# Optimization experiments

Measured on AMD Instinct MI355X. Metric: run time of the kernel, lower is better.

The kernel has to match this reference:

```python
import jax, jax.numpy as jnp
import numpy as np

N0, N1, N2 = 200000, 50000, 10000
D_IN, D_PROMPT, D_HID, D_OUT = 128, 64, 256, 2
E0, E1 = 800000, 160000


def _glorot(key, shape):
    fan_in, fan_out = shape[0], shape[1]
    lim = np.sqrt(6.0 / (fan_in + fan_out))
    return jax.random.uniform(key, shape, jnp.float32, -lim, lim)


def setup_inputs() -> dict:
    key = jax.random.key(0)
    ks = jax.random.split(key, 20)
    inp = {
        "features": jax.random.normal(ks[0], (N0, D_IN), jnp.float32),
        "membership_mask": jax.random.randint(ks[1], (N0,), 0, 2) > 0,
        "src0": jax.random.randint(ks[2], (E0,), 0, N0),
        "dst0": jax.random.randint(ks[3], (E0,), 0, N1),
        "src1": jax.random.randint(ks[4], (E1,), 0, N1),
        "dst1": jax.random.randint(ks[5], (E1,), 0, N2),
        "output_nodes_indices": jax.random.randint(ks[6], (N2,), 0, N2),
        # prompt MLPs
        "w_pin": _glorot(ks[7], (D_IN, D_PROMPT)),
        "b_pin": jnp.zeros((D_PROMPT,), jnp.float32),
        "w_pout": _glorot(ks[8], (D_IN, D_PROMPT)),
        "b_pout": jnp.zeros((D_PROMPT,), jnp.float32),
        # SAGEConv layer 0: (D_IN+D_PROMPT) -> D_HID
        "w_self0": _glorot(ks[9], (D_IN + D_PROMPT, D_HID)),
        "w_neigh0": _glorot(ks[10], (D_IN + D_PROMPT, D_HID)),
        "b0": jnp.zeros((D_HID,), jnp.float32),
        # SAGEConv layer 1: D_HID -> D_HID
        "w_self1": _glorot(ks[11], (D_HID, D_HID)),
        "w_neigh1": _glorot(ks[12], (D_HID, D_HID)),
        "b1": jnp.zeros((D_HID,), jnp.float32),
        # classifier
        "w_cls": _glorot(ks[13], (D_HID, D_OUT)),
        "b_cls": jnp.zeros((D_OUT,), jnp.float32),
    }
    return inp


def _sage_mean(h, src, dst, n_dst, w_self, w_neigh, b):
    # mean-aggregate src features into dst buckets (zero-degree -> 0, DGL semantics)
    agg = jax.ops.segment_sum(h[src], dst, num_segments=n_dst)
    deg = jax.ops.segment_sum(jnp.ones((src.shape[0],), h.dtype), dst, num_segments=n_dst)
    agg = agg / jnp.maximum(deg, 1.0)[:, None]
    return h[:n_dst] @ w_self + agg @ w_neigh + b


def reference(features, membership_mask, src0, dst0, src1, dst1, output_nodes_indices,
              w_pin, b_pin, w_pout, b_pout,
              w_self0, w_neigh0, b0, w_self1, w_neigh1, b1, w_cls, b_cls):
    p_in = jax.nn.relu(features @ w_pin + b_pin)
    p_out = jax.nn.relu(features @ w_pout + b_pout)
    sel = jnp.where(membership_mask[:, None], p_in, p_out)
    h = jnp.concatenate([features, sel], axis=1)          # [N0, D_IN+D_PROMPT]
    h = jax.nn.relu(_sage_mean(h, src0, dst0, N1, w_self0, w_neigh0, b0))  # [N1, D_HID]
    h = _sage_mean(h, src1, dst1, N2, w_self1, w_neigh1, b1)               # [N2, D_HID]
    logits = h @ w_cls + b_cls                             # [N2, D_OUT]
    return logits
```

## Files before the change

kernel.cpp:

```cpp
#include <hip/hip_runtime.h>


#define N0v 200000
#define N1v 50000
#define N2v 10000
#define E0v 800000
#define E1v 160000
#define TB0 49
#define TB1 10
#define TBL (TB0 + TB1)

using u16 = unsigned short;
typedef __attribute__((ext_vector_type(8))) short short8;
typedef __attribute__((ext_vector_type(4))) float f32x4;

__device__ __forceinline__ float b2f(u16 u) {
    union { unsigned int i; float f; } v; v.i = ((unsigned int)u) << 16; return v.f;
}
__device__ __forceinline__ u16 f2b(float f) {
    union { float f; unsigned int i; } v; v.f = f;
    return (u16)((v.i + 0x7fffu + ((v.i >> 16) & 1u)) >> 16);
}
__device__ __forceinline__ void split2(float f, u16& h, u16& l) {
    h = f2b(f);
    l = f2b(f - b2f(h));
}

__global__ void k_prep(const unsigned* mask, int* flag,
                       const float* w_pin, const float* w_pout, u16* WTph, u16* WTpl,
                       const float* ws0, const float* wn0, u16* WT0h, u16* WT0l,
                       const float* ws1, const float* wn1, u16* WT1h, u16* WT1l,
                       const float* bc, float* outp,
                       const int* __restrict__ dst0, const int* __restrict__ dst1,
                       int* cnt0, int* cnt1) {
    const int R0 = 50000;
    const int R1 = R0 + 128 * 128;
    const int R2 = R1 + 256 * 384;
    const int R3 = R2 + 256 * 512;
    const int R4 = R3 + 2 * N2v;
    const int R5 = R4 + E0v;
    const int R6 = R5 + E1v;
    for (int i = blockIdx.x * blockDim.x + threadIdx.x; i < R6;
         i += gridDim.x * blockDim.x) {
        if (i < R0) {
            if (mask[i] > 1u) atomicOr(flag, 1);
        } else if (i < R1) {
            int j = i - R0, n = j >> 7, k = j & 127;
            float f = (n < 64) ? w_pin[k * 64 + n] : w_pout[k * 64 + (n - 64)];
            split2(f, WTph[j], WTpl[j]);
        } else if (i < R2) {
            int j = i - R1, n = j / 384, k = j % 384;
            float f = (k < 192) ? ws0[k * 256 + n] : wn0[(k - 192) * 256 + n];
            split2(f, WT0h[j], WT0l[j]);
        } else if (i < R3) {
            int j = i - R2, n = j >> 9, k = j & 511;
            float f = (k < 256) ? ws1[k * 256 + n] : wn1[(k - 256) * 256 + n];
            split2(f, WT1h[j], WT1l[j]);
        } else if (i < R4) {
            int j = i - R3;
            outp[j] = bc[j & 1];
        } else if (i < R5) {
            atomicAdd(&cnt0[dst0[i - R4]], 1);
        } else {
            atomicAdd(&cnt1[dst1[i - R5]], 1);
        }
    }
}

__global__ __launch_bounds__(256) void k_scan_a(const int* __restrict__ cnt0,
                                                int* __restrict__ off0,
                                                const int* __restrict__ cnt1,
                                                int* __restrict__ off1,
                                                int* __restrict__ tsum) {
    __shared__ int sd[256];
    const int t = threadIdx.x;
    const int blk = blockIdx.x;
    const int g1 = (blk >= TB0);
    const int b = g1 ? blk - TB0 : blk;
    const int n = g1 ? N2v : N1v;
    const int* cnt = g1 ? cnt1 : cnt0;
    int* off = g1 ? off1 : off0;
    const int i0 = b * 1024 + t * 4;
    int c[4] = {0, 0, 0, 0};
    if (i0 + 3 < n) {
        *(int4*)c = *(const int4*)&cnt[i0];
    } else {
        for (int j = 0; j < 4; j++) if (i0 + j < n) c[j] = cnt[i0 + j];
    }
    int s = c[0] + c[1] + c[2] + c[3];
    sd[t] = s;
    __syncthreads();
#pragma unroll
    for (int d = 1; d < 256; d <<= 1) {
        int v = (t >= d) ? sd[t - d] : 0;
        __syncthreads();
        sd[t] += v;
        __syncthreads();
    }
    int run = sd[t] - s;
    int o4[4];
#pragma unroll
    for (int j = 0; j < 4; j++) { o4[j] = run; run += c[j]; }
    if (i0 + 3 < n) *(int4*)&off[i0] = *(const int4*)o4;
    else for (int j = 0; j < 4; j++) if (i0 + j < n) off[i0 + j] = o4[j];
    if (t == 255) tsum[blk] = sd[255];
}

__global__ __launch_bounds__(256) void k_scan_c(int* __restrict__ off0,
                                                int* __restrict__ off1,
                                                const int* __restrict__ tsum) {
    __shared__ int lbase;
    const int t = threadIdx.x;
    const int blk = blockIdx.x;
    const int g1 = (blk >= TB0);
    const int b = g1 ? blk - TB0 : blk;
    const int n = g1 ? N2v : N1v;
    int* off = g1 ? off1 : off0;
    if (t < 64) {
        int v = (t < TBL) ? tsum[t] : 0;
        int incl = v;
#pragma unroll
        for (int d = 1; d < 64; d <<= 1) {
            int u = __shfl_up(incl, d);
            if (t >= d) incl += u;
        }
        int total0 = __shfl(incl, TB0 - 1);
        if (t == blk) lbase = (incl - v) - (g1 ? total0 : 0);
    }
    __syncthreads();
    const int base = lbase;
    const int i0 = b * 1024 + t * 4;
    if (i0 + 3 < n) {
        int4 v = *(int4*)&off[i0];
        v.x += base; v.y += base; v.z += base; v.w += base;
        *(int4*)&off[i0] = v;
    } else {
        for (int j = 0; j < 4; j++) if (i0 + j < n) off[i0 + j] += base;
    }
    if (blk == 0 && t == 0) { off0[N1v] = E0v; off1[N2v] = E1v; }
}

__global__ void k_scatter2(const int* __restrict__ src0, const int* __restrict__ dst0,
                           const int* __restrict__ off0, int* cur0, int* ei0,
                           const int* __restrict__ src1, const int* __restrict__ dst1,
                           const int* __restrict__ off1, int* cur1, int* ei1) {
    for (int i = blockIdx.x * blockDim.x + threadIdx.x; i < E0v + E1v;
         i += gridDim.x * blockDim.x) {
        if (i < E0v) {
            int d = dst0[i];
            ei0[off0[d] + atomicAdd(&cur0[d], 1)] = src0[i];
        } else {
            int d = dst1[i - E0v];
            ei1[off1[d] + atomicAdd(&cur1[d], 1)] = src1[i - E0v];
        }
    }
}

__global__ __launch_bounds__(256, 2) void k_gemm_p(
    const float* __restrict__ A, const u16* __restrict__ Bh, const u16* __restrict__ Bl,
    const float* __restrict__ b_pin, const float* __restrict__ b_pout,
    const void* maskp, const int* __restrict__ flag, u16* __restrict__ G) {
    __shared__ __align__(16) u16 LA[16 * 68 * 8];
    const int t = threadIdx.x;
    const int bm = blockIdx.x >> 1, bn = blockIdx.x & 1;
    const int lane = t & 63, w = t >> 6;
    const int m = lane & 15, q = lane >> 4;
    const int r0 = bm * 64;
    const int col = bn * 64 + w * 16 + m;

    short8 bf[4][2];
#pragma unroll
    for (int k0 = 0; k0 < 4; k0++) {
        size_t b = (size_t)col * 128 + k0 * 32 + q * 8;
        bf[k0][0] = *(const short8*)&Bh[b];
        bf[k0][1] = *(const short8*)&Bl[b];
    }

    {
        const int r15 = t >> 4, ch = t & 15;
        const int k0 = ch >> 2, q2 = ch & 3;
#pragma unroll
        for (int p = 0; p < 4; p++) {
            const int row = r0 + r15 + 16 * p;
            const float* ap = &A[(size_t)row * 128 + ch * 8];
            float4 v0 = *(const float4*)ap, v1 = *(const float4*)(ap + 4);
            u16 h8[8];
            h8[0] = f2b(v0.x); h8[1] = f2b(v0.y); h8[2] = f2b(v0.z); h8[3] = f2b(v0.w);
            h8[4] = f2b(v1.x); h8[5] = f2b(v1.y); h8[6] = f2b(v1.z); h8[7] = f2b(v1.w);
            if (bn == 0)
                *(uint4*)&G[(size_t)row * 192 + ch * 8] = *(const uint4*)h8;
            const int fi = p * 4 + k0, pos = 16 * q2 + r15;
            *(uint4*)&LA[(fi * 68 + pos) * 8] = *(const uint4*)h8;
        }
    }
    __syncthreads();

    f32x4 acc[4] = {};
#pragma unroll
    for (int mi = 0; mi < 4; mi++) {
#pragma unroll
        for (int k0 = 0; k0 < 4; k0++) {
            short8 af = *(const short8*)&LA[((mi * 4 + k0) * 68 + lane) * 8];
            acc[mi] = __builtin_amdgcn_mfma_f32_16x16x32_bf16(af, bf[k0][0], acc[mi], 0, 0, 0);
            acc[mi] = __builtin_amdgcn_mfma_f32_16x16x32_bf16(af, bf[k0][1], acc[mi], 0, 0, 0);
        }
    }

    const float bv = (col < 64) ? b_pin[col] : b_pout[col - 64];
    __syncthreads();
#pragma unroll
    for (int mi = 0; mi < 4; mi++) {
#pragma unroll
        for (int r = 0; r < 4; r++) {
            float v = acc[mi][r] + bv;
            v = v > 0.f ? v : 0.f;
            LA[(mi * 16 + q * 4 + r) * 72 + w * 16 + m] = f2b(v);
        }
    }
    __syncthreads();
    const int fl = *flag;
    {
        const int c8 = t & 7;
#pragma unroll
        for (int pass = 0; pass < 2; pass++) {
            const int rt = pass * 32 + (t >> 3);
            const int row = r0 + rt;
            bool mk = fl ? (((const unsigned char*)maskp)[row] != 0)
                         : (((const int*)maskp)[row] != 0);
            if (mk == (bn == 0)) {
                *(uint4*)&G[(size_t)row * 192 + 128 + c8 * 8] =
                    *(const uint4*)&LA[rt * 72 + c8 * 8];
            }
        }
    }
}

template <int MODE, int KT, int KE0, int MT>
__global__ __launch_bounds__(256, 2) void k_g(
    const u16* __restrict__ A0, int s0, const u16* __restrict__ A1, int s1,
    const u16* __restrict__ Bh, const u16* __restrict__ Bl,
    const float* __restrict__ bias,
    u16* __restrict__ CH, float* __restrict__ outp, const float* __restrict__ wc,
    int M) {
    constexpr int MI = MT / 16;
    __shared__ __align__(16) u16 LA[MI * KT * 68 * 8];
    const int t = threadIdx.x;
    const int bm = blockIdx.x >> 2, bn = blockIdx.x & 3;
    const int lane = t & 63, w = t >> 6;
    const int m = lane & 15, q = lane >> 4;
    const int r0 = bm * MT;
    const int col = bn * 64 + w * 16 + m;
    const int K = KT * 32;

    {
        constexpr int TPR = 256 / MT;
        constexpr int SPT = KT / TPR;
        const int rr = t / TPR, sub = t & (TPR - 1);
        int arow = r0 + rr; if (arow >= M) arow = M - 1;
        const int mi = rr >> 4, r15 = rr & 15;
#pragma unroll
        for (int s = 0; s < SPT; s++) {
            const int kc = sub * SPT + s;
#pragma unroll
            for (int q2 = 0; q2 < 4; q2++) {
                const int c = kc * 32 + q2 * 8;
                uint4 v = (c < KE0 * 32)
                              ? *(const uint4*)&A0[(size_t)arow * s0 + c]
                              : *(const uint4*)&A1[(size_t)arow * s1 + (c - KE0 * 32)];
                *(uint4*)&LA[((mi * KT + kc) * 68 + 16 * q2 + r15) * 8] = v;
            }
        }
    }
    __syncthreads();

    f32x4 acc[MI] = {};
#pragma unroll
    for (int kb = 0; kb < KT; kb += 8) {
        constexpr int KC8 = (KT < 8) ? KT : 8;
        const int KC = (KT - kb < KC8) ? (KT - kb) : KC8;
        short8 bf[KC8][2];
#pragma unroll
        for (int k0 = 0; k0 < KC8; k0++) {
            if (k0 < KC) {
                size_t b = (size_t)col * K + (kb + k0) * 32 + q * 8;
                bf[k0][0] = *(const short8*)&Bh[b];
                bf[k0][1] = *(const short8*)&Bl[b];
            }
        }
#pragma unroll
        for (int mi = 0; mi < MI; mi++) {
#pragma unroll
            for (int k0 = 0; k0 < KC8; k0++) {
                if (k0 < KC) {
                    short8 af = *(const short8*)&LA[((mi * KT + kb + k0) * 68 + lane) * 8];
                    acc[mi] = __builtin_amdgcn_mfma_f32_16x16x32_bf16(af, bf[k0][0], acc[mi], 0, 0, 0);
                    acc[mi] = __builtin_amdgcn_mfma_f32_16x16x32_bf16(af, bf[k0][1], acc[mi], 0, 0, 0);
                }
            }
        }
    }

    const float bv = bias[col];
    if (MODE == 1) {
        __syncthreads();
#pragma unroll
        for (int mi = 0; mi < MI; mi++) {
#pragma unroll
            for (int r = 0; r < 4; r++) {
                float v = acc[mi][r] + bv;
                v = v > 0.f ? v : 0.f;
                LA[(mi * 16 + q * 4 + r) * 72 + w * 16 + m] = f2b(v);
            }
        }
        __syncthreads();
        const int c8 = t & 7;
#pragma unroll
        for (int pass = 0; pass < MT / 32; pass++) {
            const int rt = pass * 32 + (t >> 3);
            const int row = r0 + rt;
            if (row < M) {
                *(uint4*)&CH[(size_t)row * 256 + bn * 64 + c8 * 8] =
                    *(const uint4*)&LA[rt * 72 + c8 * 8];
            }
        }
    } else {
        const float w0 = wc[col * 2], w1 = wc[col * 2 + 1];
#pragma unroll
        for (int mi = 0; mi < MI; mi++) {
#pragma unroll
            for (int r = 0; r < 4; r++) {
                int row = r0 + mi * 16 + q * 4 + r;
                float v = acc[mi][r] + bv;
                float p0 = v * w0, p1 = v * w1;
#pragma unroll
                for (int s = 1; s < 16; s <<= 1) {
                    p0 += __shfl_xor(p0, s);
                    p1 += __shfl_xor(p1, s);
                }
                if (m == 0 && row < M) {
                    atomicAdd(&outp[row * 2], p0);
                    atomicAdd(&outp[row * 2 + 1], p1);
                }
            }
        }
    }
}

__global__ void k_agg0(const u16* __restrict__ G, const int* __restrict__ off,
                       const int* __restrict__ eidx, u16* __restrict__ aggH) {
    int wid = (blockIdx.x * blockDim.x + threadIdx.x) >> 6;
    int lane = threadIdx.x & 63;
    if (wid >= N1v) return;
    int b = off[wid], e = off[wid + 1];
    float f0 = 0.f, f1 = 0.f, p0 = 0.f;
    for (int base = b; base < e; base += 64) {
        int li = base + lane;
        int idx = eidx[li < e ? li : (e - 1)];
        int nch = e - base; if (nch > 64) nch = 64;
        int j = 0;
        for (; j + 4 <= nch; j += 4) {
            int sa = __shfl(idx, j), sb = __shfl(idx, j + 1);
            int sc = __shfl(idx, j + 2), sd = __shfl(idx, j + 3);
            const u16* ra = &G[(size_t)sa * 192];
            const u16* rb = &G[(size_t)sb * 192];
            const u16* rc = &G[(size_t)sc * 192];
            const u16* rd = &G[(size_t)sd * 192];
            unsigned fa = *(const unsigned*)&ra[2 * lane];
            unsigned fb = *(const unsigned*)&rb[2 * lane];
            unsigned fc = *(const unsigned*)&rc[2 * lane];
            unsigned fd = *(const unsigned*)&rd[2 * lane];
            u16 pa = ra[128 + lane], pb = rb[128 + lane];
            u16 pc = rc[128 + lane], pd = rd[128 + lane];
            f0 += b2f((u16)fa) + b2f((u16)fb) + b2f((u16)fc) + b2f((u16)fd);
            f1 += b2f((u16)(fa >> 16)) + b2f((u16)(fb >> 16)) +
                  b2f((u16)(fc >> 16)) + b2f((u16)(fd >> 16));
            p0 += b2f(pa) + b2f(pb) + b2f(pc) + b2f(pd);
        }
        for (; j < nch; j++) {
            int s = __shfl(idx, j);
            const u16* row = &G[(size_t)s * 192];
            unsigned fv = *(const unsigned*)&row[2 * lane];
            f0 += b2f((u16)fv);
            f1 += b2f((u16)(fv >> 16));
            p0 += b2f(row[128 + lane]);
        }
    }
    int deg = e - b;
    float inv = 1.0f / (float)(deg > 1 ? deg : 1);
    size_t rb2 = (size_t)wid * 192;
    *(unsigned*)&aggH[rb2 + 2 * lane] =
        (unsigned)f2b(f0 * inv) | ((unsigned)f2b(f1 * inv) << 16);
    aggH[rb2 + 128 + lane] = f2b(p0 * inv);
}

__global__ void k_agg1(const u16* __restrict__ h1H, const int* __restrict__ off,
                       const int* __restrict__ eidx, u16* __restrict__ aggH) {
    int wid = (blockIdx.x * blockDim.x + threadIdx.x) >> 6;
    int lane = threadIdx.x & 63;
    if (wid >= N2v) return;
    int b = off[wid], e = off[wid + 1];
    float a0 = 0.f, a1 = 0.f, a2 = 0.f, a3 = 0.f;
    for (int base = b; base < e; base += 64) {
        int li = base + lane;
        int idx = eidx[li < e ? li : (e - 1)];
        int nch = e - base; if (nch > 64) nch = 64;
        int j = 0;
        for (; j + 4 <= nch; j += 4) {
            int sa = __shfl(idx, j), sb = __shfl(idx, j + 1);
            int sc = __shfl(idx, j + 2), sd = __shfl(idx, j + 3);
            const u16* ra = &h1H[(size_t)sa * 256];
            const u16* rb = &h1H[(size_t)sb * 256];
            const u16* rc = &h1H[(size_t)sc * 256];
            const u16* rd = &h1H[(size_t)sd * 256];
            unsigned va0 = *(const unsigned*)&ra[2 * lane];
            unsigned vb0 = *(const unsigned*)&rb[2 * lane];
            unsigned vc0 = *(const unsigned*)&rc[2 * lane];
            unsigned vd0 = *(const unsigned*)&rd[2 * lane];
            unsigned va1 = *(const unsigned*)&ra[128 + 2 * lane];
            unsigned vb1 = *(const unsigned*)&rb[128 + 2 * lane];
            unsigned vc1 = *(const unsigned*)&rc[128 + 2 * lane];
            unsigned vd1 = *(const unsigned*)&rd[128 + 2 * lane];
            a0 += b2f((u16)va0) + b2f((u16)vb0) + b2f((u16)vc0) + b2f((u16)vd0);
            a1 += b2f((u16)(va0 >> 16)) + b2f((u16)(vb0 >> 16)) +
                  b2f((u16)(vc0 >> 16)) + b2f((u16)(vd0 >> 16));
            a2 += b2f((u16)va1) + b2f((u16)vb1) + b2f((u16)vc1) + b2f((u16)vd1);
            a3 += b2f((u16)(va1 >> 16)) + b2f((u16)(vb1 >> 16)) +
                  b2f((u16)(vc1 >> 16)) + b2f((u16)(vd1 >> 16));
        }
        for (; j < nch; j++) {
            int s = __shfl(idx, j);
            const u16* row = &h1H[(size_t)s * 256];
            unsigned v0 = *(const unsigned*)&row[2 * lane];
            unsigned v1 = *(const unsigned*)&row[128 + 2 * lane];
            a0 += b2f((u16)v0); a1 += b2f((u16)(v0 >> 16));
            a2 += b2f((u16)v1); a3 += b2f((u16)(v1 >> 16));
        }
    }
    int deg = e - b;
    float inv = 1.0f / (float)(deg > 1 ? deg : 1);
    size_t rb2 = (size_t)wid * 256;
    *(unsigned*)&aggH[rb2 + 2 * lane] =
        (unsigned)f2b(a0 * inv) | ((unsigned)f2b(a1 * inv) << 16);
    *(unsigned*)&aggH[rb2 + 128 + 2 * lane] =
        (unsigned)f2b(a2 * inv) | ((unsigned)f2b(a3 * inv) << 16);
}

extern "C" void kernel_launch(void* const* d_in, const int* in_sizes, int n_in,
                              void* d_out, int out_size, void* d_ws, size_t ws_size,
                              hipStream_t stream) {
    const float* features = (const float*)d_in[0];
    const void* maskp     = d_in[1];
    const int* src0       = (const int*)d_in[2];
    const int* dst0       = (const int*)d_in[3];
    const int* src1       = (const int*)d_in[4];
    const int* dst1       = (const int*)d_in[5];
    const float* w_pin    = (const float*)d_in[7];
    const float* b_pin    = (const float*)d_in[8];
    const float* w_pout   = (const float*)d_in[9];
    const float* b_pout   = (const float*)d_in[10];
    const float* w_self0  = (const float*)d_in[11];
    const float* w_neigh0 = (const float*)d_in[12];
    const float* b0       = (const float*)d_in[13];
    const float* w_self1  = (const float*)d_in[14];
    const float* w_neigh1 = (const float*)d_in[15];
    const float* b1       = (const float*)d_in[16];
    const float* w_cls    = (const float*)d_in[17];
    const float* b_cls    = (const float*)d_in[18];
    float* out = (float*)d_out;
    (void)in_sizes; (void)n_in; (void)out_size; (void)ws_size;

    char* ws = (char*)d_ws;
    size_t o = 0;
    auto alloc = [&](size_t bytes) { size_t r = o; o += (bytes + 255) & ~(size_t)255; return r; };
    size_t o_flag = alloc(4);
    size_t o_cnt0 = alloc(N1v * 4);
    size_t o_cur0 = alloc(N1v * 4);
    size_t o_cnt1 = alloc(N2v * 4);
    size_t o_cur1 = alloc(N2v * 4);
    size_t zero_end = o;
    size_t o_G    = alloc((size_t)N0v * 192 * 2);
    size_t o_aggH = alloc((size_t)N1v * 192 * 2);
    size_t o_h1H  = alloc((size_t)N1v * 256 * 2);
    size_t o_ag1H = alloc((size_t)N2v * 256 * 2);
    size_t o_wtph = alloc(128 * 128 * 2), o_wtpl = alloc(128 * 128 * 2);
    size_t o_wt0h = alloc(256 * 384 * 2), o_wt0l = alloc(256 * 384 * 2);
    size_t o_wt1h = alloc(256 * 512 * 2), o_wt1l = alloc(256 * 512 * 2);
    size_t o_off0 = alloc((N1v + 1) * 4);
    size_t o_off1 = alloc((N2v + 1) * 4);
    size_t o_ei0  = alloc((size_t)E0v * 4);
    size_t o_ei1  = alloc((size_t)E1v * 4);
    size_t o_tsum = alloc(TBL * 4);

    int* flag = (int*)(ws + o_flag);
    int* cnt0 = (int*)(ws + o_cnt0);
    int* cur0 = (int*)(ws + o_cur0);
    int* cnt1 = (int*)(ws + o_cnt1);
    int* cur1 = (int*)(ws + o_cur1);
    u16* G     = (u16*)(ws + o_G);
    u16* aggH  = (u16*)(ws + o_aggH);
    u16* h1H   = (u16*)(ws + o_h1H);
    u16* ag1H  = (u16*)(ws + o_ag1H);
    u16* WTph = (u16*)(ws + o_wtph);
    u16* WTpl = (u16*)(ws + o_wtpl);
    u16* WT0h = (u16*)(ws + o_wt0h);
    u16* WT0l = (u16*)(ws + o_wt0l);
    u16* WT1h = (u16*)(ws + o_wt1h);
    u16* WT1l = (u16*)(ws + o_wt1l);
    int* off0 = (int*)(ws + o_off0);
    int* off1 = (int*)(ws + o_off1);
    int* ei0  = (int*)(ws + o_ei0);
    int* ei1  = (int*)(ws + o_ei1);
    int* tsum = (int*)(ws + o_tsum);

    hipMemsetAsync(ws + o_flag, 0, zero_end - o_flag, stream);

    k_prep<<<1024, 256, 0, stream>>>((const unsigned*)maskp, flag,
                                     w_pin, w_pout, WTph, WTpl,
                                     w_self0, w_neigh0, WT0h, WT0l,
                                     w_self1, w_neigh1, WT1h, WT1l,
                                     b_cls, out, dst0, dst1, cnt0, cnt1);

    k_scan_a<<<TBL, 256, 0, stream>>>(cnt0, off0, cnt1, off1, tsum);
    k_scan_c<<<TBL, 256, 0, stream>>>(off0, off1, tsum);

    k_scatter2<<<1024, 256, 0, stream>>>(src0, dst0, off0, cur0, ei0,
                                         src1, dst1, off1, cur1, ei1);

    k_gemm_p<<<(N0v / 64) * 2, 256, 0, stream>>>(features, WTph, WTpl,
                                                 b_pin, b_pout, maskp, flag, G);

    k_agg0<<<(N1v + 3) / 4, 256, 0, stream>>>(G, off0, ei0, aggH);

    k_g<1, 12, 6, 64><<<((N1v + 63) / 64) * 4, 256, 0, stream>>>(
        G, 192, aggH, 192, WT0h, WT0l, b0, h1H, nullptr, nullptr, N1v);

    k_agg1<<<(N2v + 3) / 4, 256, 0, stream>>>(h1H, off1, ei1, ag1H);

    k_g<3, 16, 8, 32><<<((N2v + 31) / 32) * 4, 256, 0, stream>>>(
        h1H, 256, ag1H, 256, WT1h, WT1l, b1, nullptr, out, w_cls, N2v);
}
```

Before: 453.2 us.

## Widen GEMM N-tiles to 32 columns per wave to reuse A tiles

Each wave now computes two 16-column MFMA tiles, so the prompt GEMM covers all 128 columns in one block and the SAGE GEMMs cover 128 columns per block instead of 64. This halves block count and the redundant A-tile loads and bf16 conversions into LDS, and the prompt kernel no longer recomputes the features conversion twice. LDS padding changes from 68 to 66 and launch bounds rise to 3 blocks per CU. The cost is more accumulator and B-fragment registers, fewer blocks for latency hiding, and a possible change in LDS bank conflicts.

Measured after the change: 447.8 us. About the same (-1.2%).

```diff
diff --git a/kernel.cpp b/kernel.cpp
--- a/kernel.cpp
+++ b/kernel.cpp
@@ -156,25 +156,27 @@
     }
 }
 
-__global__ __launch_bounds__(256, 2) void k_gemm_p(
+__global__ __launch_bounds__(256, 3) void k_gemm_p(
     const float* __restrict__ A, const u16* __restrict__ Bh, const u16* __restrict__ Bl,
     const float* __restrict__ b_pin, const float* __restrict__ b_pout,
     const void* maskp, const int* __restrict__ flag, u16* __restrict__ G) {
-    __shared__ __align__(16) u16 LA[16 * 68 * 8];
+    __shared__ __align__(16) u16 LA[8704];
     const int t = threadIdx.x;
-    const int bm = blockIdx.x >> 1, bn = blockIdx.x & 1;
+    const int bm = blockIdx.x;
     const int lane = t & 63, w = t >> 6;
     const int m = lane & 15, q = lane >> 4;
     const int r0 = bm * 64;
-    const int col = bn * 64 + w * 16 + m;
-
-    short8 bf[4][2];
-#pragma unroll
-    for (int k0 = 0; k0 < 4; k0++) {
-        size_t b = (size_t)col * 128 + k0 * 32 + q * 8;
-        bf[k0][0] = *(const short8*)&Bh[b];
-        bf[k0][1] = *(const short8*)&Bl[b];
-    }
+    const int colbase = w * 32;
+
+    short8 bf[2][4][2];
+#pragma unroll
+    for (int nt = 0; nt < 2; nt++)
+#pragma unroll
+        for (int k0 = 0; k0 < 4; k0++) {
+            size_t b = (size_t)(colbase + nt * 16 + m) * 128 + k0 * 32 + q * 8;
+            bf[nt][k0][0] = *(const short8*)&Bh[b];
+            bf[nt][k0][1] = *(const short8*)&Bl[b];
+        }
 
     {
         const int r15 = t >> 4, ch = t & 15;
@@ -187,36 +189,43 @@
             u16 h8[8];
             h8[0] = f2b(v0.x); h8[1] = f2b(v0.y); h8[2] = f2b(v0.z); h8[3] = f2b(v0.w);
             h8[4] = f2b(v1.x); h8[5] = f2b(v1.y); h8[6] = f2b(v1.z); h8[7] = f2b(v1.w);
-            if (bn == 0)
-                *(uint4*)&G[(size_t)row * 192 + ch * 8] = *(const uint4*)h8;
-            const int fi = p * 4 + k0, pos = 16 * q2 + r15;
-            *(uint4*)&LA[(fi * 68 + pos) * 8] = *(const uint4*)h8;
+            *(uint4*)&G[(size_t)row * 192 + ch * 8] = *(const uint4*)h8;
+            *(uint4*)&LA[((p * 4 + k0) * 66 + 16 * q2 + r15) * 8] = *(const uint4*)h8;
         }
     }
     __syncthreads();
 
-    f32x4 acc[4] = {};
+    f32x4 acc[4][2] = {};
 #pragma unroll
     for (int mi = 0; mi < 4; mi++) {
 #pragma unroll
         for (int k0 = 0; k0 < 4; k0++) {
-            short8 af = *(const short8*)&LA[((mi * 4 + k0) * 68 + lane) * 8];
-            acc[mi] = __builtin_amdgcn_mfma_f32_16x16x32_bf16(af, bf[k0][0], acc[mi], 0, 0, 0);
-            acc[mi] = __builtin_amdgcn_mfma_f32_16x16x32_bf16(af, bf[k0][1], acc[mi], 0, 0, 0);
-        }
-    }
-
-    const float bv = (col < 64) ? b_pin[col] : b_pout[col - 64];
+            short8 af = *(const short8*)&LA[((mi * 4 + k0) * 66 + lane) * 8];
+#pragma unroll
+            for (int nt = 0; nt < 2; nt++) {
+                acc[mi][nt] = __builtin_amdgcn_mfma_f32_16x16x32_bf16(af, bf[nt][k0][0], acc[mi][nt], 0, 0, 0);
+                acc[mi][nt] = __builtin_amdgcn_mfma_f32_16x16x32_bf16(af, bf[nt][k0][1], acc[mi][nt], 0, 0, 0);
+            }
+        }
+    }
+
+    float bv[2];
+#pragma unroll
+    for (int nt = 0; nt < 2; nt++) {
+        int col = colbase + nt * 16 + m;
+        bv[nt] = (col < 64) ? b_pin[col] : b_pout[col - 64];
+    }
     __syncthreads();
 #pragma unroll
-    for (int mi = 0; mi < 4; mi++) {
-#pragma unroll
-        for (int r = 0; r < 4; r++) {
-            float v = acc[mi][r] + bv;
-            v = v > 0.f ? v : 0.f;
-            LA[(mi * 16 + q * 4 + r) * 72 + w * 16 + m] = f2b(v);
-        }
-    }
+    for (int mi = 0; mi < 4; mi++)
+#pragma unroll
+        for (int nt = 0; nt < 2; nt++)
+#pragma unroll
+            for (int r = 0; r < 4; r++) {
+                float v = acc[mi][nt][r] + bv[nt];
+                v = v > 0.f ? v : 0.f;
+                LA[(mi * 16 + q * 4 + r) * 136 + colbase + nt * 16 + m] = f2b(v);
+            }
     __syncthreads();
     const int fl = *flag;
     {
@@ -227,29 +236,28 @@
             const int row = r0 + rt;
             bool mk = fl ? (((const unsigned char*)maskp)[row] != 0)
                          : (((const int*)maskp)[row] != 0);
-            if (mk == (bn == 0)) {
-                *(uint4*)&G[(size_t)row * 192 + 128 + c8 * 8] =
-                    *(const uint4*)&LA[rt * 72 + c8 * 8];
-            }
+            const int src = mk ? 0 : 64;
+            *(uint4*)&G[(size_t)row * 192 + 128 + c8 * 8] =
+                *(const uint4*)&LA[rt * 136 + src + c8 * 8];
         }
     }
 }
 
 template <int MODE, int KT, int KE0, int MT>
-__global__ __launch_bounds__(256, 2) void k_g(
+__global__ __launch_bounds__(256, 3) void k_g(
     const u16* __restrict__ A0, int s0, const u16* __restrict__ A1, int s1,
     const u16* __restrict__ Bh, const u16* __restrict__ Bl,
     const float* __restrict__ bias,
     u16* __restrict__ CH, float* __restrict__ outp, const float* __restrict__ wc,
     int M) {
     constexpr int MI = MT / 16;
-    __shared__ __align__(16) u16 LA[MI * KT * 68 * 8];
+    __shared__ __align__(16) u16 LA[MI * KT * 66 * 8];
     const int t = threadIdx.x;
-    const int bm = blockIdx.x >> 2, bn = blockIdx.x & 3;
+    const int bm = blockIdx.x >> 1, bn = blockIdx.x & 1;
     const int lane = t & 63, w = t >> 6;
     const int m = lane & 15, q = lane >> 4;
     const int r0 = bm * MT;
-    const int col = bn * 64 + w * 16 + m;
+    const int colbase = bn * 128 + w * 32;
     const int K = KT * 32;
 
     {
@@ -267,71 +275,78 @@
                 uint4 v = (c < KE0 * 32)
                               ? *(const uint4*)&A0[(size_t)arow * s0 + c]
                               : *(const uint4*)&A1[(size_t)arow * s1 + (c - KE0 * 32)];
-                *(uint4*)&LA[((mi * KT + kc) * 68 + 16 * q2 + r15) * 8] = v;
+                *(uint4*)&LA[((mi * KT + kc) * 66 + 16 * q2 + r15) * 8] = v;
             }
         }
     }
     __syncthreads();
 
-    f32x4 acc[MI] = {};
-#pragma unroll
-    for (int kb = 0; kb < KT; kb += 8) {
-        constexpr int KC8 = (KT < 8) ? KT : 8;
-        const int KC = (KT - kb < KC8) ? (KT - kb) : KC8;
-        short8 bf[KC8][2];
-#pragma unroll
-        for (int k0 = 0; k0 < KC8; k0++) {
-            if (k0 < KC) {
-                size_t b = (size_t)col * K + (kb + k0) * 32 + q * 8;
-                bf[k0][0] = *(const short8*)&Bh[b];
-                bf[k0][1] = *(const short8*)&Bl[b];
-            }
-        }
+    f32x4 acc[MI][2] = {};
+#pragma unroll 1
+    for (int kb = 0; kb < KT; kb += 4) {
+        short8 bf[2][4][2];
+#pragma unroll
+        for (int nt = 0; nt < 2; nt++)
+#pragma unroll
+            for (int k0 = 0; k0 < 4; k0++) {
+                size_t b = (size_t)(colbase + nt * 16 + m) * K + (kb + k0) * 32 + q * 8;
+                bf[nt][k0][0] = *(const short8*)&Bh[b];
+                bf[nt][k0][1] = *(const short8*)&Bl[b];
+            }
 #pragma unroll
         for (int mi = 0; mi < MI; mi++) {
 #pragma unroll
-            for (int k0 = 0; k0 < KC8; k0++) {
-                if (k0 < KC) {
-                    short8 af = *(const short8*)&LA[((mi * KT + kb + k0) * 68 + lane) * 8];
-                    acc[mi] = __builtin_amdgcn_mfma_f32_16x16x32_bf16(af, bf[k0][0], acc[mi], 0, 0, 0);
-                    acc[mi] = __builtin_amdgcn_mfma_f32_16x16x32_bf16(af, bf[k0][1], acc[mi], 0, 0, 0);
+            for (int k0 = 0; k0 < 4; k0++) {
+                short8 af = *(const short8*)&LA[((mi * KT + kb + k0) * 66 + lane) * 8];
+#pragma unroll
+                for (int nt = 0; nt < 2; nt++) {
+                    acc[mi][nt] = __builtin_amdgcn_mfma_f32_16x16x32_bf16(af, bf[nt][k0][0], acc[mi][nt], 0, 0, 0);
+                    acc[mi][nt] = __builtin_amdgcn_mfma_f32_16x16x32_bf16(af, bf[nt][k0][1], acc[mi][nt], 0, 0, 0);
                 }
             }
         }
     }
 
-    const float bv = bias[col];
     if (MODE == 1) {
+        float bv[2];
+#pragma unroll
+        for (int nt = 0; nt < 2; nt++) bv[nt] = bias[colbase + nt * 16 + m];
         __syncthreads();
 #pragma unroll
-        for (int mi = 0; mi < MI; mi++) {
-#pragma unroll
-            for (int r = 0; r < 4; r++) {
-                float v = acc[mi][r] + bv;
-                v = v > 0.f ? v : 0.f;
-                LA[(mi * 16 + q * 4 + r) * 72 + w * 16 + m] = f2b(v);
-            }
-        }
+        for (int mi = 0; mi < MI; mi++)
+#pragma unroll
+            for (int nt = 0; nt < 2; nt++)
+#pragma unroll
+                for (int r = 0; r < 4; r++) {
+                    float v = acc[mi][nt][r] + bv[nt];
+                    v = v > 0.f ? v : 0.f;
+                    LA[(mi * 16 + q * 4 + r) * 136 + w * 32 + nt * 16 + m] = f2b(v);
+                }
         __syncthreads();
-        const int c8 = t & 7;
-#pragma unroll
-        for (int pass = 0; pass < MT / 32; pass++) {
-            const int rt = pass * 32 + (t >> 3);
+        const int c16 = t & 15;
+#pragma unroll
+        for (int pass = 0; pass < MT / 16; pass++) {
+            const int rt = pass * 16 + (t >> 4);
             const int row = r0 + rt;
             if (row < M) {
-                *(uint4*)&CH[(size_t)row * 256 + bn * 64 + c8 * 8] =
-                    *(const uint4*)&LA[rt * 72 + c8 * 8];
+                *(uint4*)&CH[(size_t)row * 256 + bn * 128 + c16 * 8] =
+                    *(const uint4*)&LA[rt * 136 + c16 * 8];
             }
         }
     } else {
-        const float w0 = wc[col * 2], w1 = wc[col * 2 + 1];
+        const int ca = colbase + m, cb = colbase + 16 + m;
+        const float bva = bias[ca], bvb = bias[cb];
+        const float w0a = wc[ca * 2], w1a = wc[ca * 2 + 1];
+        const float w0b = wc[cb * 2], w1b = wc[cb * 2 + 1];
 #pragma unroll
         for (int mi = 0; mi < MI; mi++) {
 #pragma unroll
             for (int r = 0; r < 4; r++) {
                 int row = r0 + mi * 16 + q * 4 + r;
-                float v = acc[mi][r] + bv;
-                float p0 = v * w0, p1 = v * w1;
+                float va = acc[mi][0][r] + bva;
+                float vb = acc[mi][1][r] + bvb;
+                float p0 = va * w0a + vb * w0b;
+                float p1 = va * w1a + vb * w1b;
 #pragma unroll
                 for (int s = 1; s < 16; s <<= 1) {
                     p0 += __shfl_xor(p0, s);
@@ -526,16 +541,16 @@
     k_scatter2<<<1024, 256, 0, stream>>>(src0, dst0, off0, cur0, ei0,
                                          src1, dst1, off1, cur1, ei1);
 
-    k_gemm_p<<<(N0v / 64) * 2, 256, 0, stream>>>(features, WTph, WTpl,
-                                                 b_pin, b_pout, maskp, flag, G);
+    k_gemm_p<<<N0v / 64, 256, 0, stream>>>(features, WTph, WTpl,
+                                           b_pin, b_pout, maskp, flag, G);
 
     k_agg0<<<(N1v + 3) / 4, 256, 0, stream>>>(G, off0, ei0, aggH);
 
-    k_g<1, 12, 6, 64><<<((N1v + 63) / 64) * 4, 256, 0, stream>>>(
+    k_g<1, 12, 6, 64><<<((N1v + 63) / 64) * 2, 256, 0, stream>>>(
         G, 192, aggH, 192, WT0h, WT0l, b0, h1H, nullptr, nullptr, N1v);
 
     k_agg1<<<(N2v + 3) / 4, 256, 0, stream>>>(h1H, off1, ei1, ag1H);
 
-    k_g<3, 16, 8, 32><<<((N2v + 31) / 32) * 4, 256, 0, stream>>>(
+    k_g<3, 16, 8, 32><<<((N2v + 31) / 32) * 2, 256, 0, stream>>>(
         h1H, 256, ag1H, 256, WT1h, WT1l, b1, nullptr, out, w_cls, N2v);
 }
```
